# Kernel tuning notes

Measured on AMD Instinct MI355X. Metric: run time of the kernel, lower is better.

Reference implementation:

```python
import math
import jax, jax.numpy as jnp
import numpy as np

B, N, D = 4, 4096, 1024
H, M = 16, 64
HD = D // H  # 64
EPS = 1e-6


def favor_features(data, proj):
    # data: [B,H,N,hd], proj: [M,hd] -> [B,H,N,M]
    hd = data.shape[-1]
    m = proj.shape[0]
    dn = data / math.sqrt(hd)
    norm_sq = 0.5 * jnp.sum(dn * dn, axis=-1, keepdims=True)  # [B,H,N,1]
    comb = jnp.einsum('bhnd,md->bhnm', dn, proj) - norm_sq
    comb = comb - jnp.max(comb, axis=-1, keepdims=True)
    return jnp.exp(comb) / math.sqrt(m) + EPS


def setup_inputs() -> dict:
    key = jax.random.key(0)
    ks = jax.random.split(key, 6)
    x = jax.random.normal(ks[0], (B, N, D), dtype=jnp.float32)
    qkv_w = jax.random.normal(ks[1], (3 * D, D), dtype=jnp.float32) * (1.0 / math.sqrt(D))
    qkv_b = jnp.zeros((3 * D,), dtype=jnp.float32)
    proj_w = jax.random.normal(ks[2], (D, D), dtype=jnp.float32) * (1.0 / math.sqrt(D))
    proj_b = jnp.zeros((D,), dtype=jnp.float32)
    pm = jax.random.normal(ks[3], (M, HD), dtype=jnp.float32)
    pm = pm / jnp.linalg.norm(pm, axis=-1, keepdims=True)
    return {"x": x, "qkv_w": qkv_w, "qkv_b": qkv_b, "proj_w": proj_w,
            "proj_b": proj_b, "projection_matrix": pm}


def reference(x, qkv_w, qkv_b, proj_w, proj_b, projection_matrix):
    b, n, d = x.shape
    qkv = x @ qkv_w.T + qkv_b                      # [B,N,3D]
    qkv = qkv.reshape(b, n, 3, H, HD)
    qkv = jnp.transpose(qkv, (2, 0, 3, 1, 4))      # [3,B,H,N,hd]
    q, k, v = qkv[0], qkv[1], qkv[2]
    q_p = favor_features(q, projection_matrix)     # [B,H,N,M]
    k_p = favor_features(k, projection_matrix)     # [B,H,N,M]
    kv = jnp.einsum('bhnm,bhnv->bhmv', k_p, v)     # [B,H,M,hd]
    out = jnp.einsum('bhnm,bhmv->bhnv', q_p, kv)   # [B,H,N,hd]
    k_sum = jnp.sum(k_p, axis=2)                   # [B,H,M]
    normalizer = jnp.einsum('bhnm,bhm->bhn', q_p, k_sum)[..., None]
    out = out / (normalizer + EPS)
    out = jnp.transpose(out, (0, 2, 1, 3)).reshape(b, n, d)
    return out @ proj_w.T + proj_b
```

## Files before the change

### kernel.cpp

```cpp
#include <hip/hip_runtime.h>
#include <math.h>

#define B_  4
#define N_  4096
#define D_  1024
#define H_  16
#define HD_ 64
#define M_  64
#define TD_ 3072
#define EPS_ 1e-6f

typedef __attribute__((ext_vector_type(8))) short short8;
typedef __attribute__((ext_vector_type(4))) float floatx4;
typedef unsigned int uint32;
typedef unsigned short ushort;

__device__ __forceinline__ void cvt2(float f0, float f1, uint32& hp, uint32& lp)
{
    uint32 b0 = __float_as_uint(f0), b1 = __float_as_uint(f1);
    hp = (b1 & 0xFFFF0000u) | (b0 >> 16);
    float l0 = f0 - __uint_as_float(b0 & 0xFFFF0000u);
    float l1 = f1 - __uint_as_float(b1 & 0xFFFF0000u);
    lp = (__float_as_uint(l1) & 0xFFFF0000u) | (__float_as_uint(l0) >> 16);
}

__global__ __launch_bounds__(256) void split_kernel(
    const float* __restrict__ src, ushort* __restrict__ hi,
    ushort* __restrict__ lo, int n)
{
    size_t i = ((size_t)blockIdx.x * 256 + threadIdx.x) * 8;
    if (i >= (size_t)n) return;
    float4 f0 = *(const float4*)(src + i);
    float4 f1 = *(const float4*)(src + i + 4);
    uint4 h, l;
    cvt2(f0.x, f0.y, h.x, l.x); cvt2(f0.z, f0.w, h.y, l.y);
    cvt2(f1.x, f1.y, h.z, l.z); cvt2(f1.z, f1.w, h.w, l.w);
    *(uint4*)(hi + i) = h;
    *(uint4*)(lo + i) = l;
}

#define LDSTR 40

__global__ __launch_bounds__(256, 2) void gemm_presplit_nt_bias(
    const ushort* __restrict__ Ah, const ushort* __restrict__ Al,
    const ushort* __restrict__ Bh, const ushort* __restrict__ Bl,
    const float* __restrict__ bias, float* __restrict__ C,
    int Nx, int Kx)
{
    __shared__ __align__(16) ushort AhiS[128*LDSTR], AloS[128*LDSTR];
    __shared__ __align__(16) ushort BhiS[128*LDSTR], BloS[128*LDSTR];

    const int t    = threadIdx.x;
    const int bm   = blockIdx.y * 128, bn = blockIdx.x * 128;
    const int lane = t & 63, wave = t >> 6;
    const int wm   = wave >> 1, wn = wave & 1;
    const int l16  = lane & 15, quad = lane >> 4;
    const int r    = t >> 1;
    const int ko   = (t & 1) * 16;

    floatx4 acc[4][4];
#pragma unroll
    for (int i = 0; i < 4; i++)
#pragma unroll
        for (int j = 0; j < 4; j++) acc[i][j] = (floatx4)0.f;

    const ushort* aph = Ah + (size_t)(bm + r) * Kx + ko;
    const ushort* apl = Al + (size_t)(bm + r) * Kx + ko;
    const ushort* bph = Bh + (size_t)(bn + r) * Kx + ko;
    const ushort* bpl = Bl + (size_t)(bn + r) * Kx + ko;

    for (int k0 = 0; k0 < Kx; k0 += 32) {
        uint4 vah0 = *(const uint4*)(aph + k0);
        uint4 vah1 = *(const uint4*)(aph + k0 + 8);
        uint4 val0 = *(const uint4*)(apl + k0);
        uint4 val1 = *(const uint4*)(apl + k0 + 8);
        uint4 vbh0 = *(const uint4*)(bph + k0);
        uint4 vbh1 = *(const uint4*)(bph + k0 + 8);
        uint4 vbl0 = *(const uint4*)(bpl + k0);
        uint4 vbl1 = *(const uint4*)(bpl + k0 + 8);

        __syncthreads();

        *(uint4*)&AhiS[r*LDSTR + ko]     = vah0;
        *(uint4*)&AhiS[r*LDSTR + ko + 8] = vah1;
        *(uint4*)&AloS[r*LDSTR + ko]     = val0;
        *(uint4*)&AloS[r*LDSTR + ko + 8] = val1;
        *(uint4*)&BhiS[r*LDSTR + ko]     = vbh0;
        *(uint4*)&BhiS[r*LDSTR + ko + 8] = vbh1;
        *(uint4*)&BloS[r*LDSTR + ko]     = vbl0;
        *(uint4*)&BloS[r*LDSTR + ko + 8] = vbl1;

        __syncthreads();

        short8 ah[4], al[4], bh[4], bl[4];
#pragma unroll
        for (int mi = 0; mi < 4; mi++) {
            int row = (wm*64 + mi*16 + l16) * LDSTR + quad*8;
            ah[mi] = *(const short8*)&AhiS[row];
            al[mi] = *(const short8*)&AloS[row];
        }
#pragma unroll
        for (int ni = 0; ni < 4; ni++) {
            int row = (wn*64 + ni*16 + l16) * LDSTR + quad*8;
            bh[ni] = *(const short8*)&BhiS[row];
            bl[ni] = *(const short8*)&BloS[row];
        }
#pragma unroll
        for (int mi = 0; mi < 4; mi++)
#pragma unroll
            for (int ni = 0; ni < 4; ni++) {
                floatx4 d = acc[mi][ni];
                d = __builtin_amdgcn_mfma_f32_16x16x32_bf16(ah[mi], bh[ni], d, 0, 0, 0);
                d = __builtin_amdgcn_mfma_f32_16x16x32_bf16(al[mi], bh[ni], d, 0, 0, 0);
                d = __builtin_amdgcn_mfma_f32_16x16x32_bf16(ah[mi], bl[ni], d, 0, 0, 0);
                acc[mi][ni] = d;
            }
    }

    float bia[4];
#pragma unroll
    for (int ni = 0; ni < 4; ni++)
        bia[ni] = bias[bn + wn*64 + ni*16 + l16];
#pragma unroll
    for (int mi = 0; mi < 4; mi++)
#pragma unroll
        for (int rr = 0; rr < 4; rr++) {
            int row = bm + wm*64 + mi*16 + quad*4 + rr;
            float* crow = C + (size_t)row * Nx + bn + wn*64 + l16;
#pragma unroll
            for (int ni = 0; ni < 4; ni++)
                crow[ni*16] = acc[mi][ni][rr] + bia[ni];
        }
}

__global__ __launch_bounds__(256) void favor_features_kernel(
    const float* __restrict__ qkvb, const float* __restrict__ proj,
    float* __restrict__ qp, float* __restrict__ kp)
{
    __shared__ float  projT[64*64];
    __shared__ float4 dnbuf[4][64];
    const int t = threadIdx.x;
    const int wave = t >> 6, lane = t & 63;
    const int part = blockIdx.y;
    float* outp = (part == 0) ? qp : kp;

    for (int i = t; i < 4096; i += 256)
        projT[(i & 63) * 64 + (i >> 6)] = proj[i];
    __syncthreads();

    const int h = blockIdx.x >> 6;
    const int n0 = (blockIdx.x & 63) * 64;
    const float* src = qkvb + part * D_ + h * HD_ + lane;

    for (int iter = 0; iter < 4; iter++) {
        const int n = n0 + iter * 16 + wave * 4;
        float v0 = src[(size_t)(n+0) * TD_];
        float v1 = src[(size_t)(n+1) * TD_];
        float v2 = src[(size_t)(n+2) * TD_];
        float v3 = src[(size_t)(n+3) * TD_];
        float4 dn = make_float4(v0*0.125f, v1*0.125f, v2*0.125f, v3*0.125f);
        dnbuf[wave][lane] = dn;
        float s0 = dn.x*dn.x, s1 = dn.y*dn.y, s2 = dn.z*dn.z, s3 = dn.w*dn.w;
#pragma unroll
        for (int off = 32; off >= 1; off >>= 1) {
            s0 += __shfl_xor(s0, off, 64);
            s1 += __shfl_xor(s1, off, 64);
            s2 += __shfl_xor(s2, off, 64);
            s3 += __shfl_xor(s3, off, 64);
        }
        float c0 = -0.5f*s0, c1 = -0.5f*s1, c2 = -0.5f*s2, c3 = -0.5f*s3;
#pragma unroll
        for (int d = 0; d < 64; d++) {
            float p = projT[d*64 + lane];
            float4 q = dnbuf[wave][d];
            c0 = fmaf(q.x, p, c0);
            c1 = fmaf(q.y, p, c1);
            c2 = fmaf(q.z, p, c2);
            c3 = fmaf(q.w, p, c3);
        }
        float m0 = c0, m1 = c1, m2 = c2, m3 = c3;
#pragma unroll
        for (int off = 32; off >= 1; off >>= 1) {
            m0 = fmaxf(m0, __shfl_xor(m0, off, 64));
            m1 = fmaxf(m1, __shfl_xor(m1, off, 64));
            m2 = fmaxf(m2, __shfl_xor(m2, off, 64));
            m3 = fmaxf(m3, __shfl_xor(m3, off, 64));
        }
        float r0 = expf(c0 - m0) * 0.125f + EPS_;
        float r1 = expf(c1 - m1) * 0.125f + EPS_;
        float r2 = expf(c2 - m2) * 0.125f + EPS_;
        float r3 = expf(c3 - m3) * 0.125f + EPS_;
        size_t orow = ((size_t)h * N_ + n) * 64 + lane;
        outp[orow]       = r0;
        outp[orow + 64]  = r1;
        outp[orow + 128] = r2;
        outp[orow + 192] = r3;
    }
}

__global__ __launch_bounds__(256) void kv_partial_kernel(
    const float* __restrict__ qkvb, const float* __restrict__ kp,
    float* __restrict__ kvpart, float* __restrict__ kspart)
{
    const int t = threadIdx.x;
    const int h = blockIdx.x;
    const int c = blockIdx.y;
    const int n0 = c * 128;
    const int m0 = (t & 15) * 4;
    const int v0 = (t >> 4) * 4;

    const float* kpsrc = kp + ((size_t)h * N_ + n0) * 64 + m0;
    const float* vsrc  = qkvb + (size_t)n0 * TD_ + 2 * D_ + h * HD_ + v0;

    float acc[4][4];
#pragma unroll
    for (int i = 0; i < 4; i++)
#pragma unroll
        for (int j = 0; j < 4; j++) acc[i][j] = 0.f;
    float ks[4] = {0.f, 0.f, 0.f, 0.f};

#pragma unroll 4
    for (int n = 0; n < 128; n++) {
        float4 kq = *(const float4*)(kpsrc + (size_t)n * 64);
        float4 vq = *(const float4*)(vsrc  + (size_t)n * TD_);
        acc[0][0] = fmaf(kq.x, vq.x, acc[0][0]);
        acc[0][1] = fmaf(kq.x, vq.y, acc[0][1]);
        acc[0][2] = fmaf(kq.x, vq.z, acc[0][2]);
        acc[0][3] = fmaf(kq.x, vq.w, acc[0][3]);
        acc[1][0] = fmaf(kq.y, vq.x, acc[1][0]);
        acc[1][1] = fmaf(kq.y, vq.y, acc[1][1]);
        acc[1][2] = fmaf(kq.y, vq.z, acc[1][2]);
        acc[1][3] = fmaf(kq.y, vq.w, acc[1][3]);
        acc[2][0] = fmaf(kq.z, vq.x, acc[2][0]);
        acc[2][1] = fmaf(kq.z, vq.y, acc[2][1]);
        acc[2][2] = fmaf(kq.z, vq.z, acc[2][2]);
        acc[2][3] = fmaf(kq.z, vq.w, acc[2][3]);
        acc[3][0] = fmaf(kq.w, vq.x, acc[3][0]);
        acc[3][1] = fmaf(kq.w, vq.y, acc[3][1]);
        acc[3][2] = fmaf(kq.w, vq.z, acc[3][2]);
        acc[3][3] = fmaf(kq.w, vq.w, acc[3][3]);
        if (v0 == 0) {
            ks[0] += kq.x; ks[1] += kq.y; ks[2] += kq.z; ks[3] += kq.w;
        }
    }

    float* kvp = kvpart + (((size_t)h * 32 + c) * 4096) + m0 * 64 + v0;
#pragma unroll
    for (int i = 0; i < 4; i++)
        *(float4*)(kvp + i * 64) = make_float4(acc[i][0], acc[i][1], acc[i][2], acc[i][3]);

    if (v0 == 0) {
        float* ksp = kspart + ((size_t)h * 32 + c) * 64 + m0;
        *(float4*)ksp = make_float4(ks[0], ks[1], ks[2], ks[3]);
    }
}

__global__ __launch_bounds__(256) void kv_reduce_kernel(
    const float* __restrict__ kvpart, const float* __restrict__ kspart,
    float* __restrict__ kv, float* __restrict__ ksum)
{
    const int t = threadIdx.x;
    const int h = blockIdx.x;
    const int e0 = t * 16;

    float4 s[4];
#pragma unroll
    for (int i = 0; i < 4; i++) s[i] = make_float4(0.f, 0.f, 0.f, 0.f);
    float kss = 0.f;

    for (int c = 0; c < 32; c++) {
        const float* p = kvpart + (((size_t)h * 32 + c) * 4096) + e0;
#pragma unroll
        for (int i = 0; i < 4; i++) {
            float4 x = *(const float4*)(p + i * 4);
            s[i].x += x.x; s[i].y += x.y; s[i].z += x.z; s[i].w += x.w;
        }
        if (t < 64) kss += kspart[((size_t)h * 32 + c) * 64 + t];
    }

    float* kvo = kv + (size_t)h * 4096 + e0;
#pragma unroll
    for (int i = 0; i < 4; i++) *(float4*)(kvo + i * 4) = s[i];
    if (t < 64) ksum[h * 64 + t] = kss;
}

__global__ __launch_bounds__(256) void out_kernel(
    const float* __restrict__ qp, const float* __restrict__ kv,
    const float* __restrict__ ksum, ushort* __restrict__ attn_hi,
    ushort* __restrict__ attn_lo)
{
    __shared__ float  kvs[4096];
    __shared__ float  kss[64];
    __shared__ float4 qbuf[4][64];
    const int t = threadIdx.x, lane = t & 63, wave = t >> 6;
    const int h = blockIdx.x;
    const int n0 = blockIdx.y * 64;

    for (int i = t; i < 4096; i += 256) kvs[i] = kv[(size_t)h * 4096 + i];
    if (t < 64) kss[t] = ksum[h * 64 + t];
    __syncthreads();

    const float* qsrc = qp + (size_t)h * N_ * 64 + lane;
    const size_t dbase = h * HD_ + lane;

    for (int iter = 0; iter < 4; iter++) {
        const int n = n0 + iter * 16 + wave * 4;
        float q0 = qsrc[(size_t)(n+0) * 64];
        float q1 = qsrc[(size_t)(n+1) * 64];
        float q2 = qsrc[(size_t)(n+2) * 64];
        float q3 = qsrc[(size_t)(n+3) * 64];
        qbuf[wave][lane] = make_float4(q0, q1, q2, q3);
        float t0 = q0 * kss[lane], t1 = q1 * kss[lane];
        float t2 = q2 * kss[lane], t3 = q3 * kss[lane];
#pragma unroll
        for (int off = 32; off >= 1; off >>= 1) {
            t0 += __shfl_xor(t0, off, 64);
            t1 += __shfl_xor(t1, off, 64);
            t2 += __shfl_xor(t2, off, 64);
            t3 += __shfl_xor(t3, off, 64);
        }
        float a0 = 0.f, a1 = 0.f, a2 = 0.f, a3 = 0.f;
#pragma unroll
        for (int m = 0; m < 64; m++) {
            float kvv = kvs[m*64 + lane];
            float4 q = qbuf[wave][m];
            a0 = fmaf(q.x, kvv, a0);
            a1 = fmaf(q.y, kvv, a1);
            a2 = fmaf(q.z, kvv, a2);
            a3 = fmaf(q.w, kvv, a3);
        }
        float r[4];
        r[0] = a0 / (t0 + EPS_); r[1] = a1 / (t1 + EPS_);
        r[2] = a2 / (t2 + EPS_); r[3] = a3 / (t3 + EPS_);
#pragma unroll
        for (int i = 0; i < 4; i++) {
            uint32 bits = __float_as_uint(r[i]);
            float lof = r[i] - __uint_as_float(bits & 0xFFFF0000u);
            size_t idx = (size_t)(n + i) * D_ + dbase;
            attn_hi[idx] = (ushort)(bits >> 16);
            attn_lo[idx] = (ushort)(__float_as_uint(lof) >> 16);
        }
    }
}

extern "C" void kernel_launch(void* const* d_in, const int* in_sizes, int n_in,
                              void* d_out, int out_size, void* d_ws, size_t ws_size,
                              hipStream_t stream)
{
    const float* x      = (const float*)d_in[0];
    const float* qkv_w  = (const float*)d_in[1];
    const float* qkv_b  = (const float*)d_in[2];
    const float* proj_w = (const float*)d_in[3];
    const float* proj_b = (const float*)d_in[4];
    const float* pm     = (const float*)d_in[5];
    float* out = (float*)d_out;
    float* ws  = (float*)d_ws;

    float* qkvb   = ws;
    float* qpreg  = ws + 12582912;
    float* kpreg  = qpreg + 4194304;
    float* kvb    = kpreg + 4194304;
    float* ksum   = kvb + 65536;
    float* kvpart = ksum + 1024;
    float* kspart = kvpart + 2097152;
    float* wsplit = kspart + 32768;

    ushort* xw_hi   = (ushort*)qpreg;
    ushort* xw_lo   = xw_hi + 4194304;
    float*  qp      = qpreg;
    float*  kp      = kpreg;
    ushort* attn_hi = (ushort*)kpreg;
    ushort* attn_lo = attn_hi + 4194304;
    ushort* qkvw_hi = (ushort*)wsplit;
    ushort* qkvw_lo = qkvw_hi + 3145728;
    ushort* projw_hi= qkvw_lo + 3145728;
    ushort* projw_lo= projw_hi + 1048576;

    split_kernel<<<TD_*D_/2048, 256, 0, stream>>>(qkv_w, qkvw_hi, qkvw_lo, TD_*D_);
    split_kernel<<<D_*D_/2048,  256, 0, stream>>>(proj_w, projw_hi, projw_lo, D_*D_);

    for (int b = 0; b < B_; b++) {
        const float* xb = x + (size_t)b * N_ * D_;
        float* outb = out + (size_t)b * N_ * D_;

        split_kernel<<<N_*D_/2048, 256, 0, stream>>>(xb, xw_hi, xw_lo, N_*D_);

        dim3 g1(TD_ / 128, N_ / 128);
        gemm_presplit_nt_bias<<<g1, 256, 0, stream>>>(
            xw_hi, xw_lo, qkvw_hi, qkvw_lo, qkv_b, qkvb, TD_, D_);

        dim3 g2(1024, 2);
        favor_features_kernel<<<g2, 256, 0, stream>>>(qkvb, pm, qp, kp);

        dim3 g3(16, 32);
        kv_partial_kernel<<<g3, 256, 0, stream>>>(qkvb, kp, kvpart, kspart);
        kv_reduce_kernel<<<16, 256, 0, stream>>>(kvpart, kspart, kvb, ksum);

        dim3 g4(16, 64);
        out_kernel<<<g4, 256, 0, stream>>>(qp, kvb, ksum, attn_hi, attn_lo);

        dim3 g5(D_ / 128, N_ / 128);
        gemm_presplit_nt_bias<<<g5, 256, 0, stream>>>(
            attn_hi, attn_lo, projw_hi, projw_lo, proj_b, outb, D_, D_);
    }
}
```

Baseline: 1.083 ms.

## Add 256x256 eight-phase pipelined split-bf16 GEMM and batch GEMMs across the batch

Adds a new 512-thread GEMM kernel with 256x256 tiles. It double-buffers LDS filled through direct global-to-LDS loads, runs eight interleaved load/MFMA phases with explicit waitcnt and barriers, raises priority around the MFMA blocks, and remaps workgroup IDs. When the workspace is large enough, the QKV and output projections run once over all batches instead of per batch, which cuts launches and gives larger grids. This needs more workspace, and the hand-tuned vmcnt counts carry a risk of correctness hazards.

```diff
diff --git a/kernel.cpp b/kernel.cpp
--- a/kernel.cpp
+++ b/kernel.cpp
@@ -131,6 +131,137 @@
             for (int ni = 0; ni < 4; ni++)
                 crow[ni*16] = acc[mi][ni][rr] + bia[ni];
         }
+}
+
+__device__ __forceinline__ void gload16(const void* g, void* l)
+{
+    __builtin_amdgcn_global_load_lds(
+        (const __attribute__((address_space(1))) unsigned int*)g,
+        (__attribute__((address_space(3))) unsigned int*)l,
+        16, 0, 0);
+}
+
+#define BAR() asm volatile("s_barrier" ::: "memory")
+
+__global__ __launch_bounds__(512, 2) void gemm256_8phase(
+    const ushort* __restrict__ Ah, const ushort* __restrict__ Al,
+    const ushort* __restrict__ Bh, const ushort* __restrict__ Bl,
+    const float* __restrict__ bias, float* __restrict__ C,
+    int Nx, int Kx)
+{
+    __shared__ __align__(16) ushort lds[65536];
+
+    const int t    = threadIdx.x;
+    const int wave = t >> 6, lane = t & 63;
+    const int wm   = wave >> 2, wn = wave & 3;
+    const int l16  = lane & 15, quad = lane >> 4;
+
+    const int gx  = gridDim.x;
+    const int nwg = gx * gridDim.y;
+    int bid = blockIdx.y * gx + blockIdx.x;
+    const int cpx = nwg >> 3;
+    bid = (bid & 7) * cpx + (bid >> 3);
+    const int bm = (bid / gx) * 256;
+    const int bn = (bid % gx) * 256;
+
+    const int r0   = t >> 2;
+    const int cswz = ((((t & 3) << 4) ^ ((t & 0x18) << 1)) >> 1);
+    const size_t aOff = (size_t)(bm + r0) * Kx + cswz;
+    const size_t bOff = (size_t)(bn + r0) * Kx + cswz;
+
+    const int ucol = (quad * 8) ^ ((l16 & 6) << 2);
+    const int aRB  = (wm * 64 + l16) * 32 + ucol;
+    const int bRB  = (wn * 32 + l16) * 32 + ucol;
+
+    floatx4 acc[8][4];
+#pragma unroll
+    for (int i = 0; i < 8; i++)
+#pragma unroll
+        for (int j = 0; j < 4; j++) acc[i][j] = (floatx4)0.f;
+
+#define STAGE_A(BUF, HALF, KT) do {                                          \
+    size_t go_ = (size_t)(HALF) * 128 * Kx + (size_t)(KT) * 32;              \
+    gload16(Ah + aOff + go_, &lds[(BUF)*32768 +      (HALF)*4096 + wave*512]); \
+    gload16(Al + aOff + go_, &lds[(BUF)*32768 + 8192 + (HALF)*4096 + wave*512]); \
+} while (0)
+#define STAGE_B(BUF, HALF, KT) do {                                          \
+    size_t go_ = (size_t)(HALF) * 128 * Kx + (size_t)(KT) * 32;              \
+    gload16(Bh + bOff + go_, &lds[(BUF)*32768 + 16384 + (HALF)*4096 + wave*512]); \
+    gload16(Bl + bOff + go_, &lds[(BUF)*32768 + 24576 + (HALF)*4096 + wave*512]); \
+} while (0)
+
+    STAGE_A(0, 0, 0); STAGE_B(0, 0, 0);
+    STAGE_A(0, 1, 0); STAGE_B(0, 1, 0);
+    STAGE_A(1, 0, 1); STAGE_B(1, 0, 1);
+    asm volatile("s_waitcnt vmcnt(8)" ::: "memory");
+    BAR();
+
+#define PHASE(CUR, MQ, NQ, STAGE_STMT, VM_STMT) do {                         \
+    short8 ah_[4], al_[4], bh_[2], bl_[2];                                   \
+    const int aB_ = (CUR)*32768 + (MQ)*4096 + aRB;                           \
+    const int bB_ = (CUR)*32768 + 16384 + (NQ)*4096 + bRB;                   \
+    _Pragma("unroll")                                                        \
+    for (int mi = 0; mi < 4; mi++) {                                         \
+        ah_[mi] = *(const short8*)&lds[aB_ + mi*512];                        \
+        al_[mi] = *(const short8*)&lds[aB_ + 8192 + mi*512];                 \
+    }                                                                        \
+    _Pragma("unroll")                                                        \
+    for (int ni = 0; ni < 2; ni++) {                                         \
+        bh_[ni] = *(const short8*)&lds[bB_ + ni*512];                        \
+        bl_[ni] = *(const short8*)&lds[bB_ + 8192 + ni*512];                 \
+    }                                                                        \
+    STAGE_STMT;                                                              \
+    BAR();                                                                   \
+    asm volatile("s_waitcnt lgkmcnt(0)" ::: "memory");                       \
+    __builtin_amdgcn_sched_barrier(0);                                       \
+    __builtin_amdgcn_s_setprio(1);                                           \
+    _Pragma("unroll")                                                        \
+    for (int mi = 0; mi < 4; mi++)                                           \
+    _Pragma("unroll")                                                        \
+    for (int ni = 0; ni < 2; ni++) {                                         \
+        floatx4 d = acc[(MQ)*4 + mi][(NQ)*2 + ni];                           \
+        d = __builtin_amdgcn_mfma_f32_16x16x32_bf16(ah_[mi], bh_[ni], d, 0, 0, 0); \
+        d = __builtin_amdgcn_mfma_f32_16x16x32_bf16(al_[mi], bh_[ni], d, 0, 0, 0); \
+        d = __builtin_amdgcn_mfma_f32_16x16x32_bf16(ah_[mi], bl_[ni], d, 0, 0, 0); \
+        acc[(MQ)*4 + mi][(NQ)*2 + ni] = d;                                   \
+    }                                                                        \
+    __builtin_amdgcn_s_setprio(0);                                           \
+    __builtin_amdgcn_sched_barrier(0);                                       \
+    VM_STMT;                                                                 \
+    BAR();                                                                   \
+} while (0)
+
+    for (int kt = 0; kt < 32; kt += 2) {
+        const int k1 = kt + 1;
+        const int k2 = (kt + 2 < 32) ? kt + 2 : 31;
+        const int k3 = (kt + 3 < 32) ? kt + 3 : 31;
+        PHASE(0, 0, 0, STAGE_A(1, 1, k1), asm volatile("s_waitcnt vmcnt(6)" ::: "memory"));
+        PHASE(0, 0, 1, STAGE_B(1, 1, k1), );
+        PHASE(0, 1, 0, STAGE_A(0, 0, k2), );
+        PHASE(0, 1, 1, STAGE_B(0, 0, k2), asm volatile("s_waitcnt vmcnt(8)" ::: "memory"));
+        PHASE(1, 0, 0, STAGE_A(0, 1, k2), asm volatile("s_waitcnt vmcnt(6)" ::: "memory"));
+        PHASE(1, 0, 1, STAGE_B(0, 1, k2), );
+        PHASE(1, 1, 0, STAGE_A(1, 0, k3), );
+        PHASE(1, 1, 1, STAGE_B(1, 0, k3), asm volatile("s_waitcnt vmcnt(8)" ::: "memory"));
+    }
+
+    asm volatile("s_waitcnt vmcnt(0)" ::: "memory");
+
+#pragma unroll
+    for (int f = 0; f < 8; f++) {
+        const int row = bm + (f >> 2)*128 + wm*64 + (f & 3)*16 + quad*4;
+#pragma unroll
+        for (int g = 0; g < 4; g++) {
+            const int col = bn + (g >> 1)*128 + wn*32 + (g & 1)*16 + l16;
+            const float bb = bias[col];
+#pragma unroll
+            for (int rr = 0; rr < 4; rr++)
+                C[(size_t)(row + rr) * Nx + col] = acc[f][g][rr] + bb;
+        }
+    }
+#undef PHASE
+#undef STAGE_A
+#undef STAGE_B
 }
 
 __global__ __launch_bounds__(256) void favor_features_kernel(
@@ -356,51 +487,95 @@
     float* out = (float*)d_out;
     float* ws  = (float*)d_ws;
 
-    float* qkvb   = ws;
-    float* qpreg  = ws + 12582912;
-    float* kpreg  = qpreg + 4194304;
-    float* kvb    = kpreg + 4194304;
-    float* ksum   = kvb + 65536;
-    float* kvpart = ksum + 1024;
-    float* kspart = kvpart + 2097152;
-    float* wsplit = kspart + 32768;
-
-    ushort* xw_hi   = (ushort*)qpreg;
-    ushort* xw_lo   = xw_hi + 4194304;
-    float*  qp      = qpreg;
-    float*  kp      = kpreg;
-    ushort* attn_hi = (ushort*)kpreg;
-    ushort* attn_lo = attn_hi + 4194304;
-    ushort* qkvw_hi = (ushort*)wsplit;
-    ushort* qkvw_lo = qkvw_hi + 3145728;
-    ushort* projw_hi= qkvw_lo + 3145728;
-    ushort* projw_lo= projw_hi + 1048576;
-
-    split_kernel<<<TD_*D_/2048, 256, 0, stream>>>(qkv_w, qkvw_hi, qkvw_lo, TD_*D_);
-    split_kernel<<<D_*D_/2048,  256, 0, stream>>>(proj_w, projw_hi, projw_lo, D_*D_);
-
-    for (int b = 0; b < B_; b++) {
-        const float* xb = x + (size_t)b * N_ * D_;
-        float* outb = out + (size_t)b * N_ * D_;
-
-        split_kernel<<<N_*D_/2048, 256, 0, stream>>>(xb, xw_hi, xw_lo, N_*D_);
-
-        dim3 g1(TD_ / 128, N_ / 128);
-        gemm_presplit_nt_bias<<<g1, 256, 0, stream>>>(
-            xw_hi, xw_lo, qkvw_hi, qkvw_lo, qkv_b, qkvb, TD_, D_);
-
-        dim3 g2(1024, 2);
-        favor_features_kernel<<<g2, 256, 0, stream>>>(qkvb, pm, qp, kp);
-
-        dim3 g3(16, 32);
-        kv_partial_kernel<<<g3, 256, 0, stream>>>(qkvb, kp, kvpart, kspart);
-        kv_reduce_kernel<<<16, 256, 0, stream>>>(kvpart, kspart, kvb, ksum);
-
-        dim3 g4(16, 64);
-        out_kernel<<<g4, 256, 0, stream>>>(qp, kvb, ksum, attn_hi, attn_lo);
-
-        dim3 g5(D_ / 128, N_ / 128);
-        gemm_presplit_nt_bias<<<g5, 256, 0, stream>>>(
-            attn_hi, attn_lo, projw_hi, projw_lo, proj_b, outb, D_, D_);
-    }
-}
+    const bool big = ws_size >= 327553024ULL;
+
+    if (big) {
+        float* qkvbA  = ws;
+        float* qp     = qkvbA + 50331648;
+        float* kp     = qp + 4194304;
+        float* kvb    = kp + 4194304;
+        float* ksum   = kvb + 65536;
+        float* kvpart = ksum + 1024;
+        float* kspart = kvpart + 2097152;
+        float* axw    = kspart + 32768;
+        float* wsplit = axw + 16777216;
+
+        ushort* xw_hi    = (ushort*)axw;
+        ushort* xw_lo    = xw_hi + 16777216;
+        ushort* attn_hi  = xw_hi;
+        ushort* attn_lo  = xw_lo;
+        ushort* qkvw_hi  = (ushort*)wsplit;
+        ushort* qkvw_lo  = qkvw_hi + 3145728;
+        ushort* projw_hi = qkvw_lo + 3145728;
+        ushort* projw_lo = projw_hi + 1048576;
+
+        split_kernel<<<1536, 256, 0, stream>>>(qkv_w, qkvw_hi, qkvw_lo, TD_*D_);
+        split_kernel<<<512,  256, 0, stream>>>(proj_w, projw_hi, projw_lo, D_*D_);
+        split_kernel<<<8192, 256, 0, stream>>>(x, xw_hi, xw_lo, B_*N_*D_);
+
+        gemm256_8phase<<<dim3(12, 64), 512, 0, stream>>>(
+            xw_hi, xw_lo, qkvw_hi, qkvw_lo, qkv_b, qkvbA, TD_, D_);
+
+        for (int b = 0; b < B_; b++) {
+            const float* qkvb = qkvbA + (size_t)b * N_ * TD_;
+            dim3 g2(1024, 2);
+            favor_features_kernel<<<g2, 256, 0, stream>>>(qkvb, pm, qp, kp);
+            dim3 g3(16, 32);
+            kv_partial_kernel<<<g3, 256, 0, stream>>>(qkvb, kp, kvpart, kspart);
+            kv_reduce_kernel<<<16, 256, 0, stream>>>(kvpart, kspart, kvb, ksum);
+            dim3 g4(16, 64);
+            out_kernel<<<g4, 256, 0, stream>>>(qp, kvb, ksum,
+                attn_hi + (size_t)b * N_ * D_, attn_lo + (size_t)b * N_ * D_);
+        }
+
+        gemm256_8phase<<<dim3(4, 64), 512, 0, stream>>>(
+            attn_hi, attn_lo, projw_hi, projw_lo, proj_b, out, D_, D_);
+    } else {
+        float* qkvb   = ws;
+        float* qpreg  = ws + 12582912;
+        float* kpreg  = qpreg + 4194304;
+        float* kvb    = kpreg + 4194304;
+        float* ksum   = kvb + 65536;
+        float* kvpart = ksum + 1024;
+        float* kspart = kvpart + 2097152;
+        float* wsplit = kspart + 32768;
+
+        ushort* xw_hi   = (ushort*)qpreg;
+        ushort* xw_lo   = xw_hi + 4194304;
+        float*  qp      = qpreg;
+        float*  kp      = kpreg;
+        ushort* attn_hi = (ushort*)kpreg;
+        ushort* attn_lo = attn_hi + 4194304;
+        ushort* qkvw_hi = (ushort*)wsplit;
+        ushort* qkvw_lo = qkvw_hi + 3145728;
+        ushort* projw_hi= qkvw_lo + 3145728;
+        ushort* projw_lo= projw_hi + 1048576;
+
+        split_kernel<<<TD_*D_/2048, 256, 0, stream>>>(qkv_w, qkvw_hi, qkvw_lo, TD_*D_);
+        split_kernel<<<D_*D_/2048,  256, 0, stream>>>(proj_w, projw_hi, projw_lo, D_*D_);
+
+        for (int b = 0; b < B_; b++) {
+            const float* xb = x + (size_t)b * N_ * D_;
+            float* outb = out + (size_t)b * N_ * D_;
+
+            split_kernel<<<N_*D_/2048, 256, 0, stream>>>(xb, xw_hi, xw_lo, N_*D_);
+
+            gemm256_8phase<<<dim3(12, 16), 512, 0, stream>>>(
+                xw_hi, xw_lo, qkvw_hi, qkvw_lo, qkv_b, qkvb, TD_, D_);
+
+            dim3 g2(1024, 2);
+            favor_features_kernel<<<g2, 256, 0, stream>>>(qkvb, pm, qp, kp);
+
+            dim3 g3(16, 32);
+            kv_partial_kernel<<<g3, 256, 0, stream>>>(qkvb, kp, kvpart, kspart);
+            kv_reduce_kernel<<<16, 256, 0, stream>>>(kvpart, kspart, kvb, ksum);
+
+            dim3 g4(16, 64);
+            out_kernel<<<g4, 256, 0, stream>>>(qp, kvb, ksum, attn_hi, attn_lo);
+
+            dim3 g5(D_ / 128, N_ / 128);
+            gemm_presplit_nt_bias<<<g5, 256, 0, stream>>>(
+                attn_hi, attn_lo, projw_hi, projw_lo, proj_b, outb, D_, D_);
+        }
+    }
+}
```

After: 1.091 ms. No clear change (+0.8%).
